# Kernel tuning notes

Hardware: AMD Instinct MI355X
Metric: run time of the kernel (lower is better)

The kernel has to match this reference:

```python
import jax, jax.numpy as jnp
import numpy as np

# 4D convolution via lax.conv_general_dilated with 4 spatial dims.
# Layout: input (N, C, D, H, W, T), kernel (O, I, d, h, w, t).
DN = ('NCDHWT', 'OIDHWT', 'NCDHWT')


def conv4d(x, w, b, pad):
    # torch Conv2d/Conv4d is cross-correlation, matching lax.conv_general_dilated
    y = jax.lax.conv_general_dilated(
        x, w, window_strides=(1, 1, 1, 1),
        padding=[(pad, pad)] * 4, dimension_numbers=DN)
    return y + b.reshape(1, -1, 1, 1, 1, 1)


def _kaiming(key, shape):
    fan_out = shape[0] * int(np.prod(shape[2:]))
    std = np.sqrt(2.0 / fan_out)
    return (jax.random.normal(key, shape, dtype=jnp.float32) * std).astype(jnp.float32)


def setup_inputs() -> dict:
    key = jax.random.key(0)
    ks = jax.random.split(key, 11)
    B, W, H = 256, 16, 16
    corr = jax.random.normal(ks[0], (B, W * H, W, H), dtype=jnp.float32)
    w1 = _kaiming(ks[1], (1, 1, 17, 17, 9, 9))
    w2 = _kaiming(ks[2], (1, 1, 7, 7, 7, 7))
    w3 = _kaiming(ks[3], (1, 1, 5, 5, 5, 5))
    w4 = _kaiming(ks[4], (1, 1, 3, 3, 3, 3))
    w5 = _kaiming(ks[5], (1, 1, 8, 8, 1, 1))
    b1 = jax.random.normal(ks[6], (1,), dtype=jnp.float32) * 0.01
    b2 = jax.random.normal(ks[7], (1,), dtype=jnp.float32) * 0.01
    b3 = jax.random.normal(ks[8], (1,), dtype=jnp.float32) * 0.01
    b4 = jax.random.normal(ks[9], (1,), dtype=jnp.float32) * 0.01
    b5 = jax.random.normal(ks[10], (1,), dtype=jnp.float32) * 0.01
    return {"corr": corr, "w1": w1, "b1": b1, "w2": w2, "b2": b2,
            "w3": w3, "b3": b3, "w4": w4, "b4": b4, "w5": w5, "b5": b5}


def reference(corr, w1, b1, w2, b2, w3, b3, w4, b4, w5, b5):
    B, HW, W, H = corr.shape
    x = corr.reshape(B, 1, W, H, W, H)          # (B,1,16,16,16,16)
    x = jax.nn.relu(conv4d(x, w1, b1, 4))       # (B,1, 8, 8,16,16)
    x = jax.nn.relu(conv4d(x, w2, b2, 3))
    x = jax.nn.relu(conv4d(x, w3, b3, 2))
    x = jax.nn.relu(conv4d(x, w4, b4, 1))
    out = jax.nn.sigmoid(conv4d(x, w5, b5, 0))  # (B,1, 1, 1,16,16)
    return out.reshape(B, 1, W, H)
```

## Files before the change

kernel.cpp:

```cpp
#include <hip/hip_runtime.h>
#include <math.h>


typedef short bf16x8 __attribute__((ext_vector_type(8)));
typedef float f32x4 __attribute__((ext_vector_type(4)));
typedef unsigned int u32x4 __attribute__((ext_vector_type(4)));

#define XTS 72
#define NROWS 408
#define ZROW 384

__device__ __forceinline__ unsigned short f2bf(float f) {
  unsigned int u = __float_as_uint(f);
  u += 0x7fffu + ((u >> 16) & 1u);
  return (unsigned short)(u >> 16);
}

template <int KSZ, int PAD>
__device__ __forceinline__ void build_mid(const float* __restrict__ w,
                                          unsigned short* __restrict__ Bg, int gid) {
  const int lane = gid & 63;
  const int n_tile = (gid >> 6) & 3;
  const int chunk = (gid >> 8) & 1;
  const int tap = gid >> 9;
  const int kw = tap / KSZ, kt = tap - kw * KSZ;
  const int dh_o = n_tile * 16 + (lane & 15);
  const int d_o = dh_o >> 3, h_o = dh_o & 7;
  const int kbase = chunk * 32 + (lane >> 4) * 8;
  unsigned int pk[4];
#pragma unroll
  for (int p = 0; p < 4; ++p) {
    unsigned short half[2];
#pragma unroll
    for (int s = 0; s < 2; ++s) {
      const int k = kbase + p * 2 + s;
      const int d_i = k >> 3, h_i = k & 7;
      const int kd = d_i - d_o + PAD, kh = h_i - h_o + PAD;
      float v = 0.f;
      if (kd >= 0 && kd < KSZ && kh >= 0 && kh < KSZ)
        v = w[((kd * KSZ + kh) * KSZ + kw) * KSZ + kt];
      half[s] = f2bf(v);
    }
    pk[p] = (unsigned int)half[0] | ((unsigned int)half[1] << 16);
  }
  *(int4*)(Bg + (size_t)gid * 8) = make_int4(pk[0], pk[1], pk[2], pk[3]);
}

__global__ __launch_bounds__(256) void build_all(const float* __restrict__ w1,
                                                 const float* __restrict__ w2,
                                                 const float* __restrict__ w3,
                                                 const float* __restrict__ w4,
                                                 unsigned short* __restrict__ Bg1,
                                                 unsigned short* __restrict__ Bg2,
                                                 unsigned short* __restrict__ Bg3,
                                                 unsigned short* __restrict__ Bg4) {
  const int bid = blockIdx.x, tid = threadIdx.x;
  if (bid < 648) {
    const int gid = bid * 256 + tid;
    const int lane = gid & 63;
    const int n_tile = (gid >> 6) & 3;
    const int chunk = (gid >> 8) & 7;
    const int kwkt = gid >> 11;
    const int kw = kwkt / 9, kt = kwkt - kw * 9;
    const int dh_o = n_tile * 16 + (lane & 15);
    const int d_o = dh_o >> 3, h_o = dh_o & 7;
    const int kbase = chunk * 32 + (lane >> 4) * 8;
    unsigned int pk[4];
#pragma unroll
    for (int p = 0; p < 4; ++p) {
      unsigned short half[2];
#pragma unroll
      for (int s = 0; s < 2; ++s) {
        const int k = kbase + p * 2 + s;
        const int d_i = k >> 4, h_i = k & 15;
        const int kd = d_i - d_o + 4, kh = h_i - h_o + 4;
        float v = 0.f;
        if (kd >= 0 && kd < 17 && kh >= 0 && kh < 17)
          v = w1[((kd * 17 + kh) * 9 + kw) * 9 + kt];
        half[s] = f2bf(v);
      }
      pk[p] = (unsigned int)half[0] | ((unsigned int)half[1] << 16);
    }
    *(int4*)(Bg1 + (size_t)gid * 8) = make_int4(pk[0], pk[1], pk[2], pk[3]);
  } else if (bid < 746) {
    build_mid<7, 3>(w2, Bg2, (bid - 648) * 256 + tid);
  } else if (bid < 796) {
    build_mid<5, 2>(w3, Bg3, (bid - 746) * 256 + tid);
  } else {
    build_mid<3, 1>(w4, Bg4, (bid - 796) * 256 + tid);
  }
}

__global__ __launch_bounds__(256) void conv_l1_mfma(const float* __restrict__ x,
                                                    const unsigned short* __restrict__ Bg,
                                                    float* __restrict__ P) {
  __shared__ __align__(16) unsigned short XT[NROWS * XTS];
  const int bx = blockIdx.x;
  const int b = bx >> 2, q = bx & 3;
  const int tid = threadIdx.x;
  const int lane = tid & 63, wave = tid >> 6;
  const int quad = lane >> 4, tl = lane & 15;
  const float* xb = x + (size_t)b * 65536;
  f32x4 acc[4][4] = {};

  for (int j = tid; j < (NROWS * XTS) / 8; j += 256)
    *(int4*)&XT[j * 8] = make_int4(0, 0, 0, 0);
  __syncthreads();

#pragma unroll
  for (int it = 0; it < 8; ++it) {
    const int i = tid + it * 256;
    const int dhp = i >> 6, wtq = i & 63;
    const int r0 = (wtq >> 2) * 24 + (wtq & 3) * 4 + 4;
    const float4 ra = *(const float4*)(xb + (size_t)(q * 64 + 2 * dhp) * 256 + wtq * 4);
    const float4 rb = *(const float4*)(xb + (size_t)(q * 64 + 2 * dhp + 1) * 256 + wtq * 4);
    const float a0[4] = {ra.x, ra.y, ra.z, ra.w};
    const float a1[4] = {rb.x, rb.y, rb.z, rb.w};
#pragma unroll
    for (int j = 0; j < 4; ++j) {
      const unsigned int p = (unsigned int)f2bf(a0[j]) | ((unsigned int)f2bf(a1[j]) << 16);
      *(unsigned int*)&XT[(r0 + j) * XTS + dhp * 2] = p;
    }
  }
  __syncthreads();

  const int chbase = q * 2;
  const unsigned short* Bt = Bg + (size_t)chbase * 2048 + lane * 8;
  for (int kw = 0; kw < 9; ++kw) {
    int ab[4];
#pragma unroll
    for (int m = 0; m < 4; ++m) {
      const int w_i = wave * 4 + m + kw - 4;
      const int rb = ((unsigned)w_i < 16u ? w_i * 24 : ZROW) + tl;
      ab[m] = rb * XTS + quad * 8;
    }
#pragma unroll
    for (int kt = 0; kt < 9; ++kt) {
      bf16x8 A[8], B[8];
#pragma unroll
      for (int c = 0; c < 2; ++c)
#pragma unroll
        for (int m = 0; m < 4; ++m)
          A[c * 4 + m] = *(const bf16x8*)&XT[ab[m] + kt * XTS + c * 32];
#pragma unroll
      for (int c = 0; c < 2; ++c)
#pragma unroll
        for (int n = 0; n < 4; ++n)
          B[c * 4 + n] = *(const bf16x8*)(Bt + (size_t)kt * 16384 + c * 2048 + n * 512);
#pragma unroll
      for (int c = 0; c < 2; ++c)
#pragma unroll
        for (int m = 0; m < 4; ++m)
#pragma unroll
          for (int n = 0; n < 4; ++n)
            acc[m][n] = __builtin_amdgcn_mfma_f32_16x16x32_bf16(A[c * 4 + m], B[c * 4 + n],
                                                                acc[m][n], 0, 0, 0);
    }
    Bt += 9 * 16384;
  }

  float* Pb = P + (size_t)(q * 256 + b) * 16384;
#pragma unroll
  for (int m = 0; m < 4; ++m)
#pragma unroll
    for (int n = 0; n < 4; ++n) {
      const int dh_o = n * 16 + tl;
      const int wt0 = wave * 64 + m * 16 + quad * 4;
      *(float4*)&Pb[(size_t)dh_o * 256 + wt0] = *(const float4*)&acc[m][n];
    }
}

template <int KSZ, int PAD>
__device__ __forceinline__ void run_layer(unsigned short* XT,
                                          const unsigned short* __restrict__ Bg,
                                          const float bias, int mw, int nh, int lane,
                                          int quad, int tl) {
  f32x4 acc[4][2] = {};
  const unsigned short* Bt = Bg + lane * 8;
  for (int kw = 0; kw < KSZ; ++kw) {
    int ab[4];
#pragma unroll
    for (int m = 0; m < 4; ++m) {
      const int w_i = mw * 4 + m + kw - PAD;
      const int rb = ((unsigned)w_i < 16u ? w_i * 24 : ZROW) + tl + (4 - PAD);
      ab[m] = rb * XTS + quad * 8;
    }
#pragma unroll
    for (int kt = 0; kt < KSZ; ++kt) {
      bf16x8 A[8], B[4];
#pragma unroll
      for (int c = 0; c < 2; ++c)
#pragma unroll
        for (int m = 0; m < 4; ++m)
          A[c * 4 + m] = *(const bf16x8*)&XT[ab[m] + kt * XTS + c * 32];
#pragma unroll
      for (int c = 0; c < 2; ++c)
#pragma unroll
        for (int n = 0; n < 2; ++n)
          B[c * 2 + n] =
              *(const bf16x8*)(Bt + (size_t)kt * 4096 + c * 2048 + (nh * 2 + n) * 512);
#pragma unroll
      for (int c = 0; c < 2; ++c)
#pragma unroll
        for (int m = 0; m < 4; ++m)
#pragma unroll
          for (int n = 0; n < 2; ++n)
            acc[m][n] = __builtin_amdgcn_mfma_f32_16x16x32_bf16(A[c * 4 + m], B[c * 2 + n],
                                                                acc[m][n], 0, 0, 0);
    }
    Bt += (size_t)KSZ * 4096;
  }
  __syncthreads();
#pragma unroll
  for (int m = 0; m < 4; ++m) {
    const int rbase = (mw * 4 + m) * 24 + quad * 4 + 4;
#pragma unroll
    for (int n = 0; n < 2; ++n) {
      const int col = (nh * 2 + n) * 16 + tl;
#pragma unroll
      for (int j = 0; j < 4; ++j)
        XT[(rbase + j) * XTS + col] = f2bf(fmaxf(acc[m][n][j] + bias, 0.f));
    }
  }
  __syncthreads();
}

__global__ __launch_bounds__(512) void tail_fused(const float* __restrict__ P,
                                                  const unsigned short* __restrict__ Bg2,
                                                  const unsigned short* __restrict__ Bg3,
                                                  const unsigned short* __restrict__ Bg4,
                                                  const float* __restrict__ b1,
                                                  const float* __restrict__ b2,
                                                  const float* __restrict__ b3,
                                                  const float* __restrict__ b4,
                                                  const float* __restrict__ w5,
                                                  const float* __restrict__ b5,
                                                  float* __restrict__ out) {
  __shared__ __align__(16) unsigned short XT[NROWS * XTS];
  const int b = blockIdx.x;
  const int tid = threadIdx.x;
  const int lane = tid & 63, wave = tid >> 6;
  const int quad = lane >> 4, tl = lane & 15;
  const int mw = wave >> 1, nh = wave & 1;
  const float* p0 = P + (size_t)b * 16384;
  const float* p1 = p0 + (size_t)256 * 16384;
  const float* p2 = p0 + (size_t)512 * 16384;
  const float* p3 = p0 + (size_t)768 * 16384;
  const float bias1 = b1[0];

  for (int j = tid; j < (NROWS * XTS) / 8; j += 512)
    *(int4*)&XT[j * 8] = make_int4(0, 0, 0, 0);
  __syncthreads();

#pragma unroll
  for (int it = 0; it < 4; ++it) {
    const int i = tid + it * 512;
    const int dhp = i >> 6, wtq = i & 63;
    const int r0 = (wtq >> 2) * 24 + (wtq & 3) * 4 + 4;
    const size_t off0 = (size_t)(2 * dhp) * 256 + wtq * 4;
    const float4 r0a = *(const float4*)(p0 + off0);
    const float4 r0b = *(const float4*)(p1 + off0);
    const float4 r0c = *(const float4*)(p2 + off0);
    const float4 r0d = *(const float4*)(p3 + off0);
    const float4 r1a = *(const float4*)(p0 + off0 + 256);
    const float4 r1b = *(const float4*)(p1 + off0 + 256);
    const float4 r1c = *(const float4*)(p2 + off0 + 256);
    const float4 r1d = *(const float4*)(p3 + off0 + 256);
    float a0[4] = {r0a.x + r0b.x + r0c.x + r0d.x, r0a.y + r0b.y + r0c.y + r0d.y,
                   r0a.z + r0b.z + r0c.z + r0d.z, r0a.w + r0b.w + r0c.w + r0d.w};
    float a1[4] = {r1a.x + r1b.x + r1c.x + r1d.x, r1a.y + r1b.y + r1c.y + r1d.y,
                   r1a.z + r1b.z + r1c.z + r1d.z, r1a.w + r1b.w + r1c.w + r1d.w};
#pragma unroll
    for (int j = 0; j < 4; ++j) {
      const unsigned short lo = f2bf(fmaxf(a0[j] + bias1, 0.f));
      const unsigned short hi = f2bf(fmaxf(a1[j] + bias1, 0.f));
      const unsigned int p = (unsigned int)lo | ((unsigned int)hi << 16);
      *(unsigned int*)&XT[(r0 + j) * XTS + dhp * 2] = p;
    }
  }
  __syncthreads();

  run_layer<7, 3>(XT, Bg2, b2[0], mw, nh, lane, quad, tl);
  run_layer<5, 2>(XT, Bg3, b3[0], mw, nh, lane, quad, tl);
  run_layer<3, 1>(XT, Bg4, b4[0], mw, nh, lane, quad, tl);

  if (tid < 256) {
    const int wt = tid;
    const int r = (wt >> 4) * 24 + (wt & 15) + 4;
    float s = b5[0];
    const unsigned short* row = &XT[r * XTS];
#pragma unroll
    for (int k8 = 0; k8 < 8; ++k8) {
      const u32x4 v = *(const u32x4*)&row[k8 * 8];
      const unsigned int uu[4] = {(unsigned int)v.x, (unsigned int)v.y, (unsigned int)v.z,
                                  (unsigned int)v.w};
#pragma unroll
      for (int p = 0; p < 4; ++p) {
        const float lo = __uint_as_float(uu[p] << 16);
        const float hi = __uint_as_float(uu[p] & 0xFFFF0000u);
        s += lo * w5[k8 * 8 + p * 2] + hi * w5[k8 * 8 + p * 2 + 1];
      }
    }
    out[(size_t)b * 256 + wt] = 1.f / (1.f + expf(-s));
  }
}

extern "C" void kernel_launch(void* const* d_in, const int* in_sizes, int n_in,
                              void* d_out, int out_size, void* d_ws, size_t ws_size,
                              hipStream_t stream) {
  const float* corr = (const float*)d_in[0];
  const float* w1 = (const float*)d_in[1];
  const float* b1 = (const float*)d_in[2];
  const float* w2 = (const float*)d_in[3];
  const float* b2 = (const float*)d_in[4];
  const float* w3 = (const float*)d_in[5];
  const float* b3 = (const float*)d_in[6];
  const float* w4 = (const float*)d_in[7];
  const float* b4 = (const float*)d_in[8];
  const float* w5 = (const float*)d_in[9];
  const float* b5 = (const float*)d_in[10];

  float* P = (float*)d_ws;
  unsigned short* Bg1 = (unsigned short*)((char*)d_ws + (64u << 20));
  unsigned short* Bg2 = Bg1 + (size_t)81 * 8 * 4 * 64 * 8;
  unsigned short* Bg3 = Bg2 + (size_t)49 * 2 * 4 * 64 * 8;
  unsigned short* Bg4 = Bg3 + (size_t)25 * 2 * 4 * 64 * 8;

  build_all<<<814, 256, 0, stream>>>(w1, w2, w3, w4, Bg1, Bg2, Bg3, Bg4);
  conv_l1_mfma<<<1024, 256, 0, stream>>>(corr, Bg1, P);
  tail_fused<<<256, 512, 0, stream>>>(P, Bg2, Bg3, Bg4, b1, b2, b3, b4, w5, b5,
                                      (float*)d_out);
}
```

Baseline: 313.4 us.

## Swizzle LDS activation tile and double tail kernel threads to 1024

Replaces the padded LDS row stride (72) with an unpadded 64-wide layout whose columns are XOR-swizzled by row, to avoid bank conflicts while shrinking shared memory. The tail kernel now launches 1024 threads per block, with each wave covering two M tiles instead of four in the mid layers, which halves the accumulators per thread and doubles the waves per block. The extra waves are meant to hide LDS and MFMA latency, at the cost of more barrier participants and repeated B-fragment loads per wave. The swizzle is applied consistently to stores, MFMA operand loads and the final reduction.

```diff
diff --git a/kernel.cpp b/kernel.cpp
--- a/kernel.cpp
+++ b/kernel.cpp
@@ -6,9 +6,13 @@
 typedef float f32x4 __attribute__((ext_vector_type(4)));
 typedef unsigned int u32x4 __attribute__((ext_vector_type(4)));
 
-#define XTS 72
-#define NROWS 408
+#define XTS 64
+#define NROWS 396
 #define ZROW 384
+
+__device__ __forceinline__ int xts(int row, int col) {
+  return row * XTS + (col ^ ((row & 7) << 3));
+}
 
 __device__ __forceinline__ unsigned short f2bf(float f) {
   unsigned int u = __float_as_uint(f);
@@ -119,29 +123,31 @@
 #pragma unroll
     for (int j = 0; j < 4; ++j) {
       const unsigned int p = (unsigned int)f2bf(a0[j]) | ((unsigned int)f2bf(a1[j]) << 16);
-      *(unsigned int*)&XT[(r0 + j) * XTS + dhp * 2] = p;
+      *(unsigned int*)&XT[xts(r0 + j, dhp * 2)] = p;
     }
   }
   __syncthreads();
 
   const int chbase = q * 2;
   const unsigned short* Bt = Bg + (size_t)chbase * 2048 + lane * 8;
+  const int col0 = quad * 8, col1 = quad * 8 + 32;
   for (int kw = 0; kw < 9; ++kw) {
-    int ab[4];
+    int ar[4];
 #pragma unroll
     for (int m = 0; m < 4; ++m) {
       const int w_i = wave * 4 + m + kw - 4;
-      const int rb = ((unsigned)w_i < 16u ? w_i * 24 : ZROW) + tl;
-      ab[m] = rb * XTS + quad * 8;
+      ar[m] = ((unsigned)w_i < 16u) ? (w_i * 24 + tl) : ZROW;
     }
 #pragma unroll
     for (int kt = 0; kt < 9; ++kt) {
       bf16x8 A[8], B[8];
 #pragma unroll
-      for (int c = 0; c < 2; ++c)
-#pragma unroll
-        for (int m = 0; m < 4; ++m)
-          A[c * 4 + m] = *(const bf16x8*)&XT[ab[m] + kt * XTS + c * 32];
+      for (int m = 0; m < 4; ++m) {
+        const int row = ar[m] + kt;
+        const int sw = (row & 7) << 3;
+        A[m] = *(const bf16x8*)&XT[row * XTS + (col0 ^ sw)];
+        A[4 + m] = *(const bf16x8*)&XT[row * XTS + (col1 ^ sw)];
+      }
 #pragma unroll
       for (int c = 0; c < 2; ++c)
 #pragma unroll
@@ -175,24 +181,26 @@
                                           const unsigned short* __restrict__ Bg,
                                           const float bias, int mw, int nh, int lane,
                                           int quad, int tl) {
-  f32x4 acc[4][2] = {};
+  f32x4 acc[2][2] = {};
   const unsigned short* Bt = Bg + lane * 8;
+  const int col0 = quad * 8, col1 = quad * 8 + 32;
   for (int kw = 0; kw < KSZ; ++kw) {
-    int ab[4];
-#pragma unroll
-    for (int m = 0; m < 4; ++m) {
-      const int w_i = mw * 4 + m + kw - PAD;
-      const int rb = ((unsigned)w_i < 16u ? w_i * 24 : ZROW) + tl + (4 - PAD);
-      ab[m] = rb * XTS + quad * 8;
+    int ar[2];
+#pragma unroll
+    for (int m = 0; m < 2; ++m) {
+      const int w_i = mw * 2 + m + kw - PAD;
+      ar[m] = ((unsigned)w_i < 16u) ? (w_i * 24 + tl + (4 - PAD)) : ZROW;
     }
 #pragma unroll
     for (int kt = 0; kt < KSZ; ++kt) {
-      bf16x8 A[8], B[4];
-#pragma unroll
-      for (int c = 0; c < 2; ++c)
-#pragma unroll
-        for (int m = 0; m < 4; ++m)
-          A[c * 4 + m] = *(const bf16x8*)&XT[ab[m] + kt * XTS + c * 32];
+      bf16x8 A[4], B[4];
+#pragma unroll
+      for (int m = 0; m < 2; ++m) {
+        const int row = ar[m] + kt;
+        const int sw = (row & 7) << 3;
+        A[m] = *(const bf16x8*)&XT[row * XTS + (col0 ^ sw)];
+        A[2 + m] = *(const bf16x8*)&XT[row * XTS + (col1 ^ sw)];
+      }
 #pragma unroll
       for (int c = 0; c < 2; ++c)
 #pragma unroll
@@ -202,40 +210,40 @@
 #pragma unroll
       for (int c = 0; c < 2; ++c)
 #pragma unroll
-        for (int m = 0; m < 4; ++m)
+        for (int m = 0; m < 2; ++m)
 #pragma unroll
           for (int n = 0; n < 2; ++n)
-            acc[m][n] = __builtin_amdgcn_mfma_f32_16x16x32_bf16(A[c * 4 + m], B[c * 2 + n],
+            acc[m][n] = __builtin_amdgcn_mfma_f32_16x16x32_bf16(A[c * 2 + m], B[c * 2 + n],
                                                                 acc[m][n], 0, 0, 0);
     }
     Bt += (size_t)KSZ * 4096;
   }
   __syncthreads();
 #pragma unroll
-  for (int m = 0; m < 4; ++m) {
-    const int rbase = (mw * 4 + m) * 24 + quad * 4 + 4;
+  for (int m = 0; m < 2; ++m) {
+    const int rbase = (mw * 2 + m) * 24 + quad * 4 + 4;
 #pragma unroll
     for (int n = 0; n < 2; ++n) {
       const int col = (nh * 2 + n) * 16 + tl;
 #pragma unroll
       for (int j = 0; j < 4; ++j)
-        XT[(rbase + j) * XTS + col] = f2bf(fmaxf(acc[m][n][j] + bias, 0.f));
-    }
-  }
-  __syncthreads();
-}
-
-__global__ __launch_bounds__(512) void tail_fused(const float* __restrict__ P,
-                                                  const unsigned short* __restrict__ Bg2,
-                                                  const unsigned short* __restrict__ Bg3,
-                                                  const unsigned short* __restrict__ Bg4,
-                                                  const float* __restrict__ b1,
-                                                  const float* __restrict__ b2,
-                                                  const float* __restrict__ b3,
-                                                  const float* __restrict__ b4,
-                                                  const float* __restrict__ w5,
-                                                  const float* __restrict__ b5,
-                                                  float* __restrict__ out) {
+        XT[xts(rbase + j, col)] = f2bf(fmaxf(acc[m][n][j] + bias, 0.f));
+    }
+  }
+  __syncthreads();
+}
+
+__global__ __launch_bounds__(1024) void tail_fused(const float* __restrict__ P,
+                                                   const unsigned short* __restrict__ Bg2,
+                                                   const unsigned short* __restrict__ Bg3,
+                                                   const unsigned short* __restrict__ Bg4,
+                                                   const float* __restrict__ b1,
+                                                   const float* __restrict__ b2,
+                                                   const float* __restrict__ b3,
+                                                   const float* __restrict__ b4,
+                                                   const float* __restrict__ w5,
+                                                   const float* __restrict__ b5,
+                                                   float* __restrict__ out) {
   __shared__ __align__(16) unsigned short XT[NROWS * XTS];
   const int b = blockIdx.x;
   const int tid = threadIdx.x;
@@ -248,13 +256,13 @@
   const float* p3 = p0 + (size_t)768 * 16384;
   const float bias1 = b1[0];
 
-  for (int j = tid; j < (NROWS * XTS) / 8; j += 512)
+  for (int j = tid; j < (NROWS * XTS) / 8; j += 1024)
     *(int4*)&XT[j * 8] = make_int4(0, 0, 0, 0);
   __syncthreads();
 
 #pragma unroll
-  for (int it = 0; it < 4; ++it) {
-    const int i = tid + it * 512;
+  for (int it = 0; it < 2; ++it) {
+    const int i = tid + it * 1024;
     const int dhp = i >> 6, wtq = i & 63;
     const int r0 = (wtq >> 2) * 24 + (wtq & 3) * 4 + 4;
     const size_t off0 = (size_t)(2 * dhp) * 256 + wtq * 4;
@@ -275,7 +283,7 @@
       const unsigned short lo = f2bf(fmaxf(a0[j] + bias1, 0.f));
       const unsigned short hi = f2bf(fmaxf(a1[j] + bias1, 0.f));
       const unsigned int p = (unsigned int)lo | ((unsigned int)hi << 16);
-      *(unsigned int*)&XT[(r0 + j) * XTS + dhp * 2] = p;
+      *(unsigned int*)&XT[xts(r0 + j, dhp * 2)] = p;
     }
   }
   __syncthreads();
@@ -288,10 +296,9 @@
     const int wt = tid;
     const int r = (wt >> 4) * 24 + (wt & 15) + 4;
     float s = b5[0];
-    const unsigned short* row = &XT[r * XTS];
 #pragma unroll
     for (int k8 = 0; k8 < 8; ++k8) {
-      const u32x4 v = *(const u32x4*)&row[k8 * 8];
+      const u32x4 v = *(const u32x4*)&XT[xts(r, k8 * 8)];
       const unsigned int uu[4] = {(unsigned int)v.x, (unsigned int)v.y, (unsigned int)v.z,
                                   (unsigned int)v.w};
 #pragma unroll
@@ -328,6 +335,6 @@
 
   build_all<<<814, 256, 0, stream>>>(w1, w2, w3, w4, Bg1, Bg2, Bg3, Bg4);
   conv_l1_mfma<<<1024, 256, 0, stream>>>(corr, Bg1, P);
-  tail_fused<<<256, 512, 0, stream>>>(P, Bg2, Bg3, Bg4, b1, b2, b3, b4, w5, b5,
-                                      (float*)d_out);
-}
+  tail_fused<<<256, 1024, 0, stream>>>(P, Bg2, Bg3, Bg4, b1, b2, b3, b4, w5, b5,
+                                       (float*)d_out);
+}
```

Measured after the change: 301.3 us. -3.8%, faster.
